# Kernel tuning notes

Measured on AMD Instinct MI355X. Metric: run time of the kernel, lower is better.

The kernel has to match this reference:

```python
import jax, jax.numpy as jnp
import numpy as np

CYCLE_THRESHOLD = 0.0025
LOSSFEATMULT = 1.0
EPS = 1e-6


def grid_sample(img, grid):
    """torch.nn.functional.grid_sample, mode='bilinear', align_corners=False, zero padding.
    img: [B,C,H,W]; grid: [B,Ho,Wo,2] with (x,y) in [-1,1]. Returns [B,C,Ho,Wo]."""
    B, C, H, W = img.shape
    x = (grid[..., 0] + 1.0) * (W * 0.5) - 0.5
    y = (grid[..., 1] + 1.0) * (H * 0.5) - 0.5
    x0 = jnp.floor(x)
    y0 = jnp.floor(y)
    wx = x - x0
    wy = y - y0
    x0i = x0.astype(jnp.int32)
    y0i = y0.astype(jnp.int32)

    def corner(ix, iy, w):
        valid = (ix >= 0) & (ix < W) & (iy >= 0) & (iy < H)
        ixc = jnp.clip(ix, 0, W - 1)
        iyc = jnp.clip(iy, 0, H - 1)
        v = jax.vmap(lambda im, yy, xx: im[:, yy, xx])(img, iyc, ixc)  # [B,C,Ho,Wo]
        return v * (w * valid.astype(img.dtype))[:, None]

    return (corner(x0i, y0i, (1 - wx) * (1 - wy))
            + corner(x0i + 1, y0i, wx * (1 - wy))
            + corner(x0i, y0i + 1, (1 - wx) * wy)
            + corner(x0i + 1, y0i + 1, wx * wy))


def reproject(from_l, depth, from_K, from_c2w, to_K, to_c2w):
    """Unproject pixels of the 'from' camera with depth, transform to the 'to' camera,
    project with its intrinsics. from_l: [B,H,W,2] in [-1,1]; depth: [B,1,H,W];
    K: [B,3,3]; c2w: [B,3,4]. Returns (to_l [B,H,W,2], depth_to [B,1,H,W], valid [B,1,H,W])."""
    B, H, W, _ = from_l.shape
    px = (from_l[..., 0] + 1.0) * 0.5 * W
    py = (from_l[..., 1] + 1.0) * 0.5 * H
    pix = jnp.stack([px, py, jnp.ones_like(px)], axis=-1)  # [B,H,W,3]
    Kinv = jnp.linalg.inv(from_K)
    cam = jnp.einsum('bij,bhwj->bhwi', Kinv, pix) * depth[:, 0, :, :, None]
    R_f, t_f = from_c2w[:, :, :3], from_c2w[:, :, 3]
    world = jnp.einsum('bij,bhwj->bhwi', R_f, cam) + t_f[:, None, None, :]
    R_t, t_t = to_c2w[:, :, :3], to_c2w[:, :, 3]
    cam2 = jnp.einsum('bji,bhwj->bhwi', R_t, world - t_t[:, None, None, :])  # R^T (x - t)
    proj = jnp.einsum('bij,bhwj->bhwi', to_K, cam2)
    z = proj[..., 2]
    zsafe = jnp.where(jnp.abs(z) > EPS, z, EPS)
    u = proj[..., 0] / zsafe
    v = proj[..., 1] / zsafe
    to_l = jnp.stack([u / W * 2.0 - 1.0, v / H * 2.0 - 1.0], axis=-1)
    return to_l, z[:, None], z > EPS


def _forward(features1, features2, depth1, depth2, mask1, mask2, K1, K2, c2w1, c2w2):
    B, C, H, W = features1.shape
    dt = features1.dtype
    # identity grid at pixel centers, normalized to [-1,1] (matches (pts+0.5)/size*2-1)
    xs = (jnp.arange(W, dtype=dt) + 0.5) / W * 2.0 - 1.0
    ys = (jnp.arange(H, dtype=dt) + 0.5) / H * 2.0 - 1.0
    gx, gy = jnp.meshgrid(xs, ys)  # [H,W]
    l1 = jnp.broadcast_to(jnp.stack([gx, gy], axis=-1)[None], (B, H, W, 2))
    l2 = l1
    l2_1, _, _ = reproject(l2, depth2, K2, c2w2, K1, c2w1)
    l1_2, _, _ = reproject(l1, depth1, K1, c2w1, K2, c2w2)
    # cycle consistency: warp l2->1 coords by l1->2
    l1_2_1 = grid_sample(l2_1.transpose(0, 3, 1, 2), l1_2).transpose(0, 2, 3, 1)
    dist1 = jnp.sqrt(jax.lax.stop_gradient(((l1 - l1_2_1) ** 2).sum(-1)))[:, None]  # [B,1,H,W]
    f1 = grid_sample(features1, l1)
    f2 = grid_sample(features2, l2)
    f1_2 = grid_sample(features2, l1_2)
    f2_1 = grid_sample(features1, l2_1)
    weights1 = (dist1 < CYCLE_THRESHOLD).astype(dt) * mask1
    lossfeat1 = ((f1 - f1_2) ** 2).sum(1, keepdims=True) * weights1
    # NOTE: original source multiplies lossfeat2 by weights1 (not weights2); replicated faithfully.
    lossfeat2 = ((f2 - f2_1) ** 2).sum(1, keepdims=True) * weights1
    return LOSSFEATMULT * (lossfeat1.mean() + lossfeat2.mean())


def setup_inputs():
    key = jax.random.key(0)
    ks = jax.random.split(key, 6)
    B, C, H, W = 1, 64, 512, 512
    features1 = jax.random.normal(ks[0], (B, C, H, W), jnp.float32)
    features2 = jax.random.normal(ks[1], (B, C, H, W), jnp.float32)
    image1 = jax.random.uniform(ks[2], (B, 3, H, W), jnp.float32)
    image2 = jax.random.uniform(ks[3], (B, 3, H, W), jnp.float32)
    depth1 = 2.0 + 4.0 * jax.random.uniform(ks[4], (B, 1, H, W), jnp.float32)
    depth2 = 2.0 + 4.0 * jax.random.uniform(ks[5], (B, 1, H, W), jnp.float32)
    mask1 = jnp.ones((B, 1, H, W), jnp.float32)
    mask2 = jnp.ones((B, 1, H, W), jnp.float32)
    f = 400.0
    K = jnp.array([[[f, 0.0, W / 2.0], [0.0, f, H / 2.0], [0.0, 0.0, 1.0]]], jnp.float32)
    c2w1 = jnp.concatenate([jnp.eye(3, dtype=jnp.float32), jnp.zeros((3, 1), jnp.float32)], axis=1)[None]
    th = 0.05  # small yaw between cameras
    R2 = jnp.array([[np.cos(th), 0.0, np.sin(th)], [0.0, 1.0, 0.0], [-np.sin(th), 0.0, np.cos(th)]], jnp.float32)
    c2w2 = jnp.concatenate([R2, jnp.array([[0.2], [0.0], [0.0]], jnp.float32)], axis=1)[None]
    return dict(features1=features1, features2=features2, image1=image1, image2=image2,
                depth1=depth1, depth2=depth2, mask1=mask1, mask2=mask2,
                K1=K, K2=K, c2w1=c2w1, c2w2=c2w2)


def reference(features1, features2, image1, image2, depth1, depth2, mask1, mask2, K1, K2, c2w1, c2w2):
    # images are only used for visualization in the original; they do not affect the loss
    return _forward(features1, features2, depth1, depth2, mask1, mask2, K1, K2, c2w1, c2w2)
```

## Files before the change

kernel.cpp:

```cpp
#include <hip/hip_runtime.h>

#define WW 512
#define HH 512
#define CC 64
#define HW (HH*WW)
#define PPB 128
#define NBLK (HW/PPB)

typedef float f2v __attribute__((ext_vector_type(2), aligned(4)));

struct __align__(16) LItem {
    float4 ewA;
    float4 ewB;
    int4   o;
    float  wgt;
    int    pix;
    int    pad0, pad1;
};

__device__ __forceinline__ void invert3(const float* __restrict__ m, float* o) {
    float a = m[0], b = m[1], c = m[2];
    float d = m[3], e = m[4], f = m[5];
    float g = m[6], h = m[7], i = m[8];
    float C11 =  (e*i - f*h);
    float C12 = -(d*i - f*g);
    float C13 =  (d*h - e*g);
    float C21 = -(b*i - c*h);
    float C22 =  (a*i - c*g);
    float C23 = -(a*h - b*g);
    float C31 =  (b*f - c*e);
    float C32 = -(a*f - c*d);
    float C33 =  (a*e - b*d);
    float det = a*C11 + b*C12 + c*C13;
    float id = 1.0f / det;
    o[0] = C11*id; o[1] = C21*id; o[2] = C31*id;
    o[3] = C12*id; o[4] = C22*id; o[5] = C32*id;
    o[6] = C13*id; o[7] = C23*id; o[8] = C33*id;
}

__device__ __forceinline__ void reproj_pt(
    float px, float py, float d,
    const float Kinv[9],
    const float* __restrict__ cf, const float* __restrict__ ct,
    const float* __restrict__ Kt,
    float& ox, float& oy)
{
    float cx = Kinv[0]*px + Kinv[1]*py + Kinv[2];
    float cy = Kinv[3]*px + Kinv[4]*py + Kinv[5];
    float cz = Kinv[6]*px + Kinv[7]*py + Kinv[8];
    cx *= d; cy *= d; cz *= d;
    float wx = cf[0]*cx + cf[1]*cy + cf[2]*cz + cf[3];
    float wy = cf[4]*cx + cf[5]*cy + cf[6]*cz + cf[7];
    float wz = cf[8]*cx + cf[9]*cy + cf[10]*cz + cf[11];
    float qx = wx - ct[3], qy = wy - ct[7], qz = wz - ct[11];
    float ax = ct[0]*qx + ct[4]*qy + ct[8]*qz;
    float ay = ct[1]*qx + ct[5]*qy + ct[9]*qz;
    float az = ct[2]*qx + ct[6]*qy + ct[10]*qz;
    float p0 = Kt[0]*ax + Kt[1]*ay + Kt[2]*az;
    float p1 = Kt[3]*ax + Kt[4]*ay + Kt[5]*az;
    float p2 = Kt[6]*ax + Kt[7]*ay + Kt[8]*az;
    float zs = (fabsf(p2) > 1e-6f) ? p2 : 1e-6f;
    float u = p0 / zs;
    float v = p1 / zs;
    ox = u / 512.0f * 2.0f - 1.0f;
    oy = v / 512.0f * 2.0f - 1.0f;
}

__device__ __forceinline__ void bilin_state(
    float lx, float ly, float4& ew, int& o0, int& o1)
{
    float xf = (lx + 1.0f) * 256.0f - 0.5f;
    float yf = (ly + 1.0f) * 256.0f - 0.5f;
    float x0 = floorf(xf), y0 = floorf(yf);
    float wx = xf - x0, wy = yf - y0;
    x0 = fminf(fmaxf(x0, -1e8f), 1e8f);
    y0 = fminf(fmaxf(y0, -1e8f), 1e8f);
    int x0i = (int)x0, y0i = (int)y0;

    float vx0 = (x0i >= 0 && x0i < WW) ? 1.0f : 0.0f;
    float vx1 = (x0i + 1 >= 0 && x0i + 1 < WW) ? 1.0f : 0.0f;
    float vy0 = (y0i >= 0 && y0i < HH) ? 1.0f : 0.0f;
    float vy1 = (y0i + 1 >= 0 && y0i + 1 < HH) ? 1.0f : 0.0f;
    float w00 = (1.0f - wx) * (1.0f - wy) * vx0 * vy0;
    float w10 = wx * (1.0f - wy) * vx1 * vy0;
    float w01 = (1.0f - wx) * wy * vx0 * vy1;
    float w11 = wx * wy * vx1 * vy1;

    int xc = min(max(x0i, 0), WW - 2);
    float e0r0 = (xc == x0i) ? w00 : ((xc == x0i + 1) ? w10 : 0.0f);
    float e1r0 = (xc + 1 == x0i + 1) ? w10 : ((xc + 1 == x0i) ? w00 : 0.0f);
    float e0r1 = (xc == x0i) ? w01 : ((xc == x0i + 1) ? w11 : 0.0f);
    float e1r1 = (xc + 1 == x0i + 1) ? w11 : ((xc + 1 == x0i) ? w01 : 0.0f);
    ew = make_float4(e0r0, e1r0, e0r1, e1r1);
    o0 = min(max(y0i, 0), HH - 1) * WW + xc;
    o1 = min(max(y0i + 1, 0), HH - 1) * WW + xc;
}

__global__ __launch_bounds__(256) void fused_kernel(
    const float* __restrict__ f1, const float* __restrict__ f2,
    const float* __restrict__ d1p, const float* __restrict__ d2p,
    const float* __restrict__ m1p,
    const float* __restrict__ K1, const float* __restrict__ K2,
    const float* __restrict__ cw1, const float* __restrict__ cw2,
    float* __restrict__ out)
{
    __shared__ LItem items[PPB];
    __shared__ int nitems;
    __shared__ float sred[4];

    int bid = (int)(blockIdx.x & 7) * (NBLK / 8) + (int)(blockIdx.x >> 3);

    int tid  = threadIdx.x;
    int wave = tid >> 6;
    int lane = tid & 63;
    bool active = tid < PPB;
    int pix  = bid * PPB + (tid & (PPB - 1));
    int j = pix & (WW - 1);
    int i = pix >> 9;

    if (tid == 0) nitems = 0;

    float wgt = 0.0f;
    float4 ewA; int a0 = 0, a1 = 0;
    float l21x = 0.0f, l21y = 0.0f;
    if (active) {
        float Ki1[9], Ki2[9];
        invert3(K1, Ki1);
        invert3(K2, Ki2);
        float px = j + 0.5f, py = i + 0.5f;

        float l12x, l12y;
        reproj_pt(px, py, d1p[pix], Ki1, cw1, cw2, K2, l12x, l12y);
        reproj_pt(px, py, d2p[pix], Ki2, cw2, cw1, K1, l21x, l21y);

        bilin_state(l12x, l12y, ewA, a0, a1);

        f2v cdr0 = *(const f2v*)(d2p + a0);
        f2v cdr1 = *(const f2v*)(d2p + a1);
        int co[4] = {a0, a0 + 1, a1, a1 + 1};
        float cw[4] = {ewA.x, ewA.y, ewA.z, ewA.w};
        float cds[4] = {cdr0.x, cdr0.y, cdr1.x, cdr1.y};
        float vx = 0.0f, vy = 0.0f;
        #pragma unroll
        for (int k = 0; k < 4; ++k) {
            int cj = co[k] & (WW - 1), ci = co[k] >> 9;
            float cxv, cyv;
            reproj_pt(cj + 0.5f, ci + 0.5f, cds[k], Ki2, cw2, cw1, K1, cxv, cyv);
            vx += cw[k] * cxv;
            vy += cw[k] * cyv;
        }
        float gx = (j + 0.5f) / 512.0f * 2.0f - 1.0f;
        float gy = (i + 0.5f) / 512.0f * 2.0f - 1.0f;
        float ddx = gx - vx, ddy = gy - vy;
        float dist = sqrtf(ddx * ddx + ddy * ddy);
        wgt = (dist < 0.0025f) ? m1p[pix] : 0.0f;
    }

    __syncthreads();

    if (active && wgt != 0.0f) {
        float4 ewB; int b0, b1;
        bilin_state(l21x, l21y, ewB, b0, b1);
        int slot = atomicAdd(&nitems, 1);
        LItem s;
        s.ewA = ewA; s.ewB = ewB;
        s.o = make_int4(a0, a1, b0, b1);
        s.wgt = wgt; s.pix = pix; s.pad0 = 0; s.pad1 = 0;
        items[slot] = s;
    }
    __syncthreads();

    int n = nitems;
    int isub = lane >> 4;
    int c16  = lane & 15;

    float lsum = 0.0f;
    for (int base = wave * 4; base < n; base += 16) {
        int it = base + isub;
        bool has = it < n;
        int idx = has ? it : (n - 1);

        float4 eA = items[idx].ewA;
        float4 eB = items[idx].ewB;
        int4   o  = items[idx].o;
        float  w  = has ? items[idx].wgt : 0.0f;
        int    p  = items[idx].pix;

        float acc = 0.0f;
        #pragma unroll
        for (int chunk = 0; chunk < 4; ++chunk) {
            const float* F1 = f1 + (size_t)(chunk * 16 + c16) * HW;
            const float* F2 = f2 + (size_t)(chunk * 16 + c16) * HW;
            f2v a01 = *(const f2v*)(F2 + o.x);
            f2v a23 = *(const f2v*)(F2 + o.y);
            f2v b01 = *(const f2v*)(F1 + o.z);
            f2v b23 = *(const f2v*)(F1 + o.w);
            float p1v = F1[p],   p2v = F2[p];

            float s1 = eA.x * a01.x + eA.y * a01.y + eA.z * a23.x + eA.w * a23.y;
            float s2 = eB.x * b01.x + eB.y * b01.y + eB.z * b23.x + eB.w * b23.y;
            float e1 = p1v - s1;
            float e2 = p2v - s2;
            acc += e1 * e1 + e2 * e2;
        }
        lsum += w * acc;
    }

    #pragma unroll
    for (int off = 32; off > 0; off >>= 1)
        lsum += __shfl_down(lsum, off);
    if (lane == 0) sred[wave] = lsum;
    __syncthreads();
    if (tid == 0) {
        float t = (sred[0] + sred[1]) + (sred[2] + sred[3]);
        if (t != 0.0f) atomicAdd(out, t * (1.0f / 262144.0f));
    }
}

extern "C" void kernel_launch(void* const* d_in, const int* in_sizes, int n_in,
                              void* d_out, int out_size, void* d_ws, size_t ws_size,
                              hipStream_t stream) {
    const float* f1  = (const float*)d_in[0];
    const float* f2  = (const float*)d_in[1];
    const float* dp1 = (const float*)d_in[4];
    const float* dp2 = (const float*)d_in[5];
    const float* m1  = (const float*)d_in[6];
    const float* K1  = (const float*)d_in[8];
    const float* K2  = (const float*)d_in[9];
    const float* c1  = (const float*)d_in[10];
    const float* c2  = (const float*)d_in[11];

    float* out = (float*)d_out;
    hipMemsetAsync(out, 0, sizeof(float), stream);
    fused_kernel<<<NBLK, 256, 0, stream>>>(
        f1, f2, dp1, dp2, m1, K1, K2, c1, c2, out);
}
```

Baseline: 48.69 us.

## Split into setup compaction kernel and channel-parallel gather kernel with fallback

Moves the per-pixel validity test and bilinear setup into a separate kernel that compacts the valid items into a global workspace list using atomics. A second kernel then spreads the gather across a 2D grid, with channel pairs on one axis and item strides on the other, so each thread reads two channels of many items instead of each block handling 64 channels for its own items. This aims to balance the sparse gather work across the GPU, at the cost of an extra launch, an extra memset and a workspace round trip. A single-kernel fallback is kept for when the workspace is too small.

```diff
diff --git a/kernel.cpp b/kernel.cpp
--- a/kernel.cpp
+++ b/kernel.cpp
@@ -6,6 +6,8 @@
 #define HW (HH*WW)
 #define PPB 128
 #define NBLK (HW/PPB)
+#define GXB 96
+#define NPAIR 32
 
 typedef float f2v __attribute__((ext_vector_type(2), aligned(4)));
 
@@ -96,23 +98,20 @@
     o1 = min(max(y0i + 1, 0), HH - 1) * WW + xc;
 }
 
-__global__ __launch_bounds__(256) void fused_kernel(
-    const float* __restrict__ f1, const float* __restrict__ f2,
+__global__ __launch_bounds__(256) void setup_kernel(
     const float* __restrict__ d1p, const float* __restrict__ d2p,
     const float* __restrict__ m1p,
     const float* __restrict__ K1, const float* __restrict__ K2,
     const float* __restrict__ cw1, const float* __restrict__ cw2,
-    float* __restrict__ out)
+    int* __restrict__ gcnt, LItem* __restrict__ comp)
 {
     __shared__ LItem items[PPB];
     __shared__ int nitems;
-    __shared__ float sred[4];
+    __shared__ int gbase;
 
     int bid = (int)(blockIdx.x & 7) * (NBLK / 8) + (int)(blockIdx.x >> 3);
 
     int tid  = threadIdx.x;
-    int wave = tid >> 6;
-    int lane = tid & 63;
     bool active = tid < PPB;
     int pix  = bid * PPB + (tid & (PPB - 1));
     int j = pix & (WW - 1);
@@ -170,50 +169,138 @@
     }
     __syncthreads();
 
-    int n = nitems;
-    int isub = lane >> 4;
-    int c16  = lane & 15;
+    if (tid == 0 && nitems > 0) gbase = atomicAdd(gcnt, nitems);
+    __syncthreads();
+
+    if (tid < nitems) comp[gbase + tid] = items[tid];
+}
+
+__global__ __launch_bounds__(256) void gather_kernel(
+    const float* __restrict__ f1, const float* __restrict__ f2,
+    const int* __restrict__ gcnt, const LItem* __restrict__ comp,
+    float* __restrict__ out)
+{
+    int count = gcnt[0];
+    int c0 = blockIdx.y * 2;
+    const float* F1a = f1 + (size_t)c0 * HW;
+    const float* F2a = f2 + (size_t)c0 * HW;
+    const float* F1b = F1a + HW;
+    const float* F2b = F2a + HW;
 
     float lsum = 0.0f;
-    for (int base = wave * 4; base < n; base += 16) {
-        int it = base + isub;
-        bool has = it < n;
-        int idx = has ? it : (n - 1);
-
-        float4 eA = items[idx].ewA;
-        float4 eB = items[idx].ewB;
-        int4   o  = items[idx].o;
-        float  w  = has ? items[idx].wgt : 0.0f;
-        int    p  = items[idx].pix;
-
-        float acc = 0.0f;
-        #pragma unroll
-        for (int chunk = 0; chunk < 4; ++chunk) {
-            const float* F1 = f1 + (size_t)(chunk * 16 + c16) * HW;
-            const float* F2 = f2 + (size_t)(chunk * 16 + c16) * HW;
-            f2v a01 = *(const f2v*)(F2 + o.x);
-            f2v a23 = *(const f2v*)(F2 + o.y);
-            f2v b01 = *(const f2v*)(F1 + o.z);
-            f2v b23 = *(const f2v*)(F1 + o.w);
-            float p1v = F1[p],   p2v = F2[p];
-
-            float s1 = eA.x * a01.x + eA.y * a01.y + eA.z * a23.x + eA.w * a23.y;
-            float s2 = eB.x * b01.x + eB.y * b01.y + eB.z * b23.x + eB.w * b23.y;
-            float e1 = p1v - s1;
-            float e2 = p2v - s2;
-            acc += e1 * e1 + e2 * e2;
-        }
-        lsum += w * acc;
+    for (int it = blockIdx.x * 256 + threadIdx.x; it < count; it += GXB * 256) {
+        const float4* c4 = (const float4*)&comp[it];
+        float4 eA = c4[0];
+        float4 eB = c4[1];
+        int4   o  = ((const int4*)c4)[2];
+        float4 t  = c4[3];
+        float  w  = t.x;
+        int    p  = __float_as_int(t.y);
+
+        f2v a01x = *(const f2v*)(F2a + o.x);
+        f2v a23x = *(const f2v*)(F2a + o.y);
+        f2v b01x = *(const f2v*)(F1a + o.z);
+        f2v b23x = *(const f2v*)(F1a + o.w);
+        float p1x = F1a[p], p2x = F2a[p];
+        f2v a01y = *(const f2v*)(F2b + o.x);
+        f2v a23y = *(const f2v*)(F2b + o.y);
+        f2v b01y = *(const f2v*)(F1b + o.z);
+        f2v b23y = *(const f2v*)(F1b + o.w);
+        float p1y = F1b[p], p2y = F2b[p];
+
+        float s1x = eA.x*a01x.x + eA.y*a01x.y + eA.z*a23x.x + eA.w*a23x.y;
+        float s2x = eB.x*b01x.x + eB.y*b01x.y + eB.z*b23x.x + eB.w*b23x.y;
+        float e1x = p1x - s1x;
+        float e2x = p2x - s2x;
+        float s1y = eA.x*a01y.x + eA.y*a01y.y + eA.z*a23y.x + eA.w*a23y.y;
+        float s2y = eB.x*b01y.x + eB.y*b01y.y + eB.z*b23y.x + eB.w*b23y.y;
+        float e1y = p1y - s1y;
+        float e2y = p2y - s2y;
+        lsum += w * (e1x*e1x + e2x*e2x + e1y*e1y + e2y*e2y);
     }
 
     #pragma unroll
     for (int off = 32; off > 0; off >>= 1)
         lsum += __shfl_down(lsum, off);
-    if (lane == 0) sred[wave] = lsum;
-    __syncthreads();
-    if (tid == 0) {
+    __shared__ float sred[4];
+    int wave = threadIdx.x >> 6;
+    if ((threadIdx.x & 63) == 0) sred[wave] = lsum;
+    __syncthreads();
+    if (threadIdx.x == 0) {
         float t = (sred[0] + sred[1]) + (sred[2] + sred[3]);
         if (t != 0.0f) atomicAdd(out, t * (1.0f / 262144.0f));
+    }
+}
+
+__global__ __launch_bounds__(256) void mono_kernel(
+    const float* __restrict__ f1, const float* __restrict__ f2,
+    const float* __restrict__ d1p, const float* __restrict__ d2p,
+    const float* __restrict__ m1p,
+    const float* __restrict__ K1, const float* __restrict__ K2,
+    const float* __restrict__ cw1, const float* __restrict__ cw2,
+    float* __restrict__ out)
+{
+    int pix = blockIdx.x * 256 + threadIdx.x;
+    int j = pix & (WW - 1);
+    int i = pix >> 9;
+    float Ki1[9], Ki2[9];
+    invert3(K1, Ki1);
+    invert3(K2, Ki2);
+    float px = j + 0.5f, py = i + 0.5f;
+
+    float l12x, l12y, l21x, l21y;
+    reproj_pt(px, py, d1p[pix], Ki1, cw1, cw2, K2, l12x, l12y);
+    reproj_pt(px, py, d2p[pix], Ki2, cw2, cw1, K1, l21x, l21y);
+
+    float4 ewA; int a0, a1;
+    bilin_state(l12x, l12y, ewA, a0, a1);
+
+    float vx = 0.0f, vy = 0.0f;
+    {
+        int co[4] = {a0, a0 + 1, a1, a1 + 1};
+        float cw[4] = {ewA.x, ewA.y, ewA.z, ewA.w};
+        #pragma unroll
+        for (int k = 0; k < 4; ++k) {
+            int cj = co[k] & (WW - 1), ci = co[k] >> 9;
+            float cxv, cyv;
+            reproj_pt(cj + 0.5f, ci + 0.5f, d2p[co[k]], Ki2, cw2, cw1, K1, cxv, cyv);
+            vx += cw[k] * cxv;
+            vy += cw[k] * cyv;
+        }
+    }
+    float gx = (j + 0.5f) / 512.0f * 2.0f - 1.0f;
+    float gy = (i + 0.5f) / 512.0f * 2.0f - 1.0f;
+    float ddx = gx - vx, ddy = gy - vy;
+    float dist = sqrtf(ddx * ddx + ddy * ddy);
+    float wgt = (dist < 0.0025f) ? m1p[pix] : 0.0f;
+
+    float lsum = 0.0f;
+    if (wgt != 0.0f) {
+        float4 ewB; int b0, b1;
+        bilin_state(l21x, l21y, ewB, b0, b1);
+        float acc = 0.0f;
+        const float* F1 = f1;
+        const float* F2 = f2;
+        for (int c = 0; c < CC; ++c) {
+            float s1 = ewA.x*F2[a0] + ewA.y*F2[a0+1] + ewA.z*F2[a1] + ewA.w*F2[a1+1];
+            float s2 = ewB.x*F1[b0] + ewB.y*F1[b0+1] + ewB.z*F1[b1] + ewB.w*F1[b1+1];
+            float e1 = F1[pix] - s1;
+            float e2 = F2[pix] - s2;
+            acc += e1 * e1 + e2 * e2;
+            F1 += HW; F2 += HW;
+        }
+        lsum = wgt * acc;
+    }
+
+    #pragma unroll
+    for (int off = 32; off > 0; off >>= 1)
+        lsum += __shfl_down(lsum, off);
+    __shared__ float sred[4];
+    if ((threadIdx.x & 63) == 0) sred[threadIdx.x >> 6] = lsum;
+    __syncthreads();
+    if (threadIdx.x == 0) {
+        float t = (sred[0] + sred[1]) + (sred[2] + sred[3]);
+        atomicAdd(out, t * (1.0f / 262144.0f));
     }
 }
 
@@ -232,6 +319,18 @@
 
     float* out = (float*)d_out;
     hipMemsetAsync(out, 0, sizeof(float), stream);
-    fused_kernel<<<NBLK, 256, 0, stream>>>(
-        f1, f2, dp1, dp2, m1, K1, K2, c1, c2, out);
-}
+
+    const size_t need = 64 + (size_t)HW * sizeof(LItem);
+    if (ws_size >= need) {
+        int* gcnt = (int*)d_ws;
+        LItem* comp = (LItem*)((char*)d_ws + 64);
+        hipMemsetAsync(gcnt, 0, sizeof(int), stream);
+        setup_kernel<<<NBLK, 256, 0, stream>>>(
+            dp1, dp2, m1, K1, K2, c1, c2, gcnt, comp);
+        gather_kernel<<<dim3(GXB, NPAIR), 256, 0, stream>>>(
+            f1, f2, gcnt, comp, out);
+    } else {
+        mono_kernel<<<HW / 256, 256, 0, stream>>>(
+            f1, f2, dp1, dp2, m1, K1, K2, c1, c2, out);
+    }
+}
```

New measurement: 80.98 us. +66.3%, slower.
